# Kernel tuning notes

Measured on AMD Instinct MI355X. Metric: run time of the kernel, lower is better.

Reference implementation:

```python
import jax, jax.numpy as jnp
import numpy as np

N_PARENT = 16384
N_CHILD = 8 * N_PARENT  # nearest upsample, nempty=False: 8 children per parent
C = 128
K = 27  # 3x3x3 octree conv stencil


def setup_inputs() -> dict:
    key = jax.random.key(0)
    k1, k2, k3, k4 = jax.random.split(key, 4)
    x = jax.random.normal(k1, (N_PARENT, C), dtype=jnp.float32)
    # conv weight per stencil offset, fan-in scaled init
    w = jax.random.normal(k2, (K, C, C), dtype=jnp.float32) / np.sqrt(K * C)
    b = jnp.zeros((C,), dtype=jnp.float32)
    # neighbor table at depth+1; -1 marks missing neighbors (zero-padded)
    neigh = jax.random.randint(k3, (N_CHILD, K), -1, N_CHILD, dtype=jnp.int32)
    return {"x": x, "w": w, "b": b, "neigh": neigh}


def reference(x, w, b, neigh):
    # OctreeUpsample(nearest, nempty=False): copy each parent feature to its
    # 8 contiguous children at depth+1.
    xu = jnp.repeat(x, 8, axis=0)  # [N_child, C]
    # OctreeConv: gather 27 neighbors (missing -> 0), then GEMM + bias.
    valid = neigh >= 0  # [N_child, 27]
    g = jnp.where(valid[..., None], xu[jnp.clip(neigh, 0)], 0.0)  # [N_child, 27, C]
    out = jnp.einsum('nkc,kcd->nd', g, w) + b  # [N_child, C]
    return out
```

## Files before the change

kernel.cpp:

```cpp
#include <hip/hip_runtime.h>
#include <hip/hip_bf16.h>

#define N_PARENT 16384
#define N_CHILD (8 * N_PARENT)
#define CC 128
#define KK 27

#define BM 256
#define BN 128
#define BK 32

#define XB_OFF 0
#define XB_ELEMS (N_PARENT * CC)
#define WT_OFF XB_ELEMS
#define WT_ELEMS (KK * CC * CC)
#define ZR_OFF (WT_OFF + WT_ELEMS)
#define ZR_ELEMS 128
#define ZR_ROW 19840

typedef __attribute__((ext_vector_type(8))) __bf16 bf16x8;
typedef __attribute__((ext_vector_type(4))) float f32x4;

__device__ __forceinline__ void gll16(const void* g, void* l) {
  __builtin_amdgcn_global_load_lds(
      (const __attribute__((address_space(1))) unsigned int*)g,
      (__attribute__((address_space(3))) unsigned int*)l,
      16, 0, 0);
}

__global__ void prep_kernel(const float* __restrict__ x,
                            const float* __restrict__ w,
                            __hip_bfloat16* __restrict__ ws) {
  const int stride = gridDim.x * blockDim.x;
  const int tid = blockIdx.x * blockDim.x + threadIdx.x;
  for (int i = tid; i < XB_ELEMS; i += stride)
    ws[XB_OFF + i] = __float2bfloat16(x[i]);
  for (int j = tid; j < WT_ELEMS; j += stride) {
    const int k = j / (CC * CC);
    const int rem = j - k * CC * CC;
    const int d = rem >> 7;
    const int c = rem & 127;
    ws[WT_OFF + j] = __float2bfloat16(w[k * CC * CC + c * CC + d]);
  }
  if (tid < ZR_ELEMS) ws[ZR_OFF + tid] = __float2bfloat16(0.0f);
}

__global__ __launch_bounds__(256, 2) void upconv_kernel(
    const int* __restrict__ neigh,
    const __hip_bfloat16* __restrict__ ws,
    const float* __restrict__ bias,
    float* __restrict__ out) {
  __shared__ __align__(16) __hip_bfloat16 As[2][BM * BK];
  __shared__ __align__(16) __hip_bfloat16 Bs[2][BN * BK];
  __shared__ unsigned short ridx[BM * KK];

  const int tid = threadIdx.x;
  const int wv = tid >> 6;
  const int l = tid & 63;
  const int wr = wv >> 1;
  const int wc = wv & 1;
  const int row0 = blockIdx.x * BM;

  for (int j = tid; j < BM * KK; j += 256) {
    const int nv = neigh[row0 * KK + j];
    ridx[j] = (unsigned short)((nv >= 0) ? (nv >> 3) : ZR_ROW);
  }
  __syncthreads();

  const int lr = l & 15;
  const int coE = (((l >> 4) ^ ((lr >> 1) & 3)) * 8);
  const int lch = ((l & 3) ^ ((l >> 3) & 3)) * 16;

  const char* xbB = (const char*)(ws + XB_OFF);
  const char* wLane =
      (const char*)(ws + WT_OFF) + (wv * 32 + (l >> 2)) * 256 + lch;

  f32x4 acc[8][4] = {};

  const int riB = (wv * 64 + (l >> 2)) * KK;
  int rr[4], nr[4];
#pragma unroll
  for (int i = 0; i < 4; ++i) rr[i] = ((int)ridx[riB + i * 16 * KK]) << 8;

  auto stageA = [&](int buf, int qb, const int* r) {
#pragma unroll
    for (int i = 0; i < 4; ++i)
      gll16(xbB + r[i] + qb + lch, &As[buf][(wv * 64 + i * 16) * BK]);
  };
  auto stageB = [&](int buf, int tqb) {
#pragma unroll
    for (int j = 0; j < 2; ++j)
      gll16(wLane + tqb + j * 4096, &Bs[buf][(wv * 32 + j * 16) * BK]);
  };

  auto compute = [&](int buf) {
    bf16x8 a[8], b[4];
#pragma unroll
    for (int m = 0; m < 8; ++m)
      a[m] = *reinterpret_cast<const bf16x8*>(
          &As[buf][(wr * 128 + m * 16 + lr) * BK + coE]);
#pragma unroll
    for (int n = 0; n < 4; ++n)
      b[n] = *reinterpret_cast<const bf16x8*>(
          &Bs[buf][(wc * 64 + n * 16 + lr) * BK + coE]);
    __builtin_amdgcn_s_setprio(1);
#pragma unroll
    for (int m = 0; m < 8; ++m)
#pragma unroll
      for (int n = 0; n < 4; ++n)
        acc[m][n] = __builtin_amdgcn_mfma_f32_16x16x32_bf16(
            a[m], b[n], acc[m][n], 0, 0, 0);
    __builtin_amdgcn_s_setprio(0);
  };

#define WAITN(n) asm volatile("s_waitcnt vmcnt(" #n ")" ::: "memory")
#define BAR() __builtin_amdgcn_s_barrier()

  stageB(0, 0);
  stageA(0, 0, rr);

  for (int k = 0; k < KK; ++k) {
    const int tb = k * 32768;

    stageB(1, tb + 64);
    stageA(1, 64, rr);
    WAITN(6); BAR();
    compute(0);
    BAR();

    stageB(0, tb + 128);
    stageA(0, 128, rr);
    WAITN(6); BAR();
    compute(1);
    BAR();

    stageB(1, tb + 192);
    stageA(1, 192, rr);
#pragma unroll
    for (int i = 0; i < 4; ++i)
      nr[i] = (k + 1 < KK) ? (((int)ridx[riB + i * 16 * KK + k + 1]) << 8)
                           : rr[i];
    WAITN(6); BAR();
    compute(0);
    BAR();

    if (k + 1 < KK) {
      stageB(0, tb + 32768);
      stageA(0, 0, nr);
      WAITN(6);
    } else {
      WAITN(0);
    }
    BAR();
    compute(1);
    BAR();

#pragma unroll
    for (int i = 0; i < 4; ++i) rr[i] = nr[i];
  }

  float bv[4];
#pragma unroll
  for (int n = 0; n < 4; ++n) bv[n] = bias[wc * 64 + n * 16 + lr];
  const int rbase = row0 + wr * 128 + (l >> 4) * 4;
#pragma unroll
  for (int m = 0; m < 8; ++m)
#pragma unroll
    for (int n = 0; n < 4; ++n)
#pragma unroll
      for (int q = 0; q < 4; ++q)
        out[(size_t)(rbase + m * 16 + q) * CC + wc * 64 + n * 16 + lr] =
            acc[m][n][q] + bv[n];
}

extern "C" void kernel_launch(void* const* d_in, const int* in_sizes, int n_in,
                              void* d_out, int out_size, void* d_ws,
                              size_t ws_size, hipStream_t stream) {
  const float* x = (const float*)d_in[0];
  const float* w = (const float*)d_in[1];
  const float* b = (const float*)d_in[2];
  const int* neigh = (const int*)d_in[3];
  __hip_bfloat16* ws = (__hip_bfloat16*)d_ws;
  float* out = (float*)d_out;

  hipLaunchKernelGGL(prep_kernel, dim3(512), dim3(256), 0, stream, x, w, ws);
  hipLaunchKernelGGL(upconv_kernel, dim3(N_CHILD / BM), dim3(256), 0, stream,
                     neigh, ws, b, out);
}
```

Measured before the change: 129.5 us.

## Precompute per-parent products for all stencil offsets, then gather-sum per child

Computes x_parent·W_k for every parent and all 27 offsets in a dense GEMM (8x fewer rows than children), storing bf16 partial products in workspace. A gather kernel then sums the 27 neighbour partials plus bias per child. This trades most of the MFMA work for a large intermediate write and a random-access gather. It also adds an extra bf16 rounding of partial products, and runs only when the workspace is big enough.

```diff
diff --git a/kernel.cpp b/kernel.cpp
--- a/kernel.cpp
+++ b/kernel.cpp
@@ -17,6 +17,11 @@
 #define ZR_OFF (WT_OFF + WT_ELEMS)
 #define ZR_ELEMS 128
 #define ZR_ROW 19840
+#define PZ_OFF (ZR_OFF + ZR_ELEMS)
+#define PZ_ELEMS (KK * CC)
+#define P_OFF (PZ_OFF + PZ_ELEMS)
+#define P_ELEMS ((size_t)N_PARENT * KK * CC)
+#define NCOL (KK * CC)
 
 typedef __attribute__((ext_vector_type(8))) __bf16 bf16x8;
 typedef __attribute__((ext_vector_type(4))) float f32x4;
@@ -30,7 +35,7 @@
 
 __global__ void prep_kernel(const float* __restrict__ x,
                             const float* __restrict__ w,
-                            __hip_bfloat16* __restrict__ ws) {
+                            __hip_bfloat16* __restrict__ ws, int zero_pz) {
   const int stride = gridDim.x * blockDim.x;
   const int tid = blockIdx.x * blockDim.x + threadIdx.x;
   for (int i = tid; i < XB_ELEMS; i += stride)
@@ -43,6 +48,122 @@
     ws[WT_OFF + j] = __float2bfloat16(w[k * CC * CC + c * CC + d]);
   }
   if (tid < ZR_ELEMS) ws[ZR_OFF + tid] = __float2bfloat16(0.0f);
+  if (zero_pz && tid < PZ_ELEMS) ws[PZ_OFF + tid] = __float2bfloat16(0.0f);
+}
+
+__global__ __launch_bounds__(256, 3) void pgemm_kernel(
+    const __hip_bfloat16* __restrict__ ws, __hip_bfloat16* __restrict__ Pout) {
+  __shared__ __align__(16) __hip_bfloat16 As[2][BM * BK];
+  __shared__ __align__(16) __hip_bfloat16 Bs[2][BN * BK];
+
+  const int tid = threadIdx.x;
+  const int wv = tid >> 6, l = tid & 63;
+  const int wr = wv >> 1, wc = wv & 1;
+  const int bm = blockIdx.x & 63;
+  const int bn = blockIdx.x >> 6;
+  const int row0 = bm * BM;
+
+  const int lr = l & 15;
+  const int coE = ((l >> 4) ^ ((lr >> 1) & 3)) * 8;
+  const int lch = ((l & 3) ^ ((l >> 3) & 3)) * 16;
+
+  const char* aLane = (const char*)(ws + XB_OFF) +
+                      (size_t)(row0 + wv * 64 + (l >> 2)) * 256 + lch;
+  const char* wLane = (const char*)(ws + WT_OFF) + bn * 32768 +
+                      (wv * 32 + (l >> 2)) * 256 + lch;
+
+  f32x4 acc[8][4] = {};
+
+  auto stageAB = [&](int buf, int qb) {
+#pragma unroll
+    for (int i = 0; i < 4; ++i)
+      gll16(aLane + i * 4096 + qb, &As[buf][(wv * 64 + i * 16) * BK]);
+#pragma unroll
+    for (int j = 0; j < 2; ++j)
+      gll16(wLane + j * 4096 + qb, &Bs[buf][(wv * 32 + j * 16) * BK]);
+  };
+  auto compute = [&](int buf) {
+    bf16x8 a[8], b[4];
+#pragma unroll
+    for (int m = 0; m < 8; ++m)
+      a[m] = *reinterpret_cast<const bf16x8*>(
+          &As[buf][(wr * 128 + m * 16 + lr) * BK + coE]);
+#pragma unroll
+    for (int n = 0; n < 4; ++n)
+      b[n] = *reinterpret_cast<const bf16x8*>(
+          &Bs[buf][(wc * 64 + n * 16 + lr) * BK + coE]);
+#pragma unroll
+    for (int m = 0; m < 8; ++m)
+#pragma unroll
+      for (int n = 0; n < 4; ++n)
+        acc[m][n] = __builtin_amdgcn_mfma_f32_16x16x32_bf16(a[m], b[n],
+                                                            acc[m][n], 0, 0, 0);
+  };
+
+#define WAITN(n) asm volatile("s_waitcnt vmcnt(" #n ")" ::: "memory")
+#define BAR() __builtin_amdgcn_s_barrier()
+
+  stageAB(0, 0);
+#pragma unroll
+  for (int q = 0; q < 4; ++q) {
+    if (q + 1 < 4) {
+      stageAB((q + 1) & 1, (q + 1) * 64);
+      WAITN(6);
+    } else {
+      WAITN(0);
+    }
+    BAR();
+    compute(q & 1);
+    BAR();
+  }
+
+  const int prow = row0 + wr * 128 + (l >> 4) * 4;
+  const int pcol = bn * 128 + wc * 64;
+#pragma unroll
+  for (int m = 0; m < 8; ++m)
+#pragma unroll
+    for (int n = 0; n < 4; ++n)
+#pragma unroll
+      for (int q = 0; q < 4; ++q)
+        Pout[(size_t)(prow + m * 16 + q) * NCOL + pcol + n * 16 + lr] =
+            __float2bfloat16(acc[m][n][q]);
+}
+
+__global__ __launch_bounds__(256, 8) void gather_kernel(
+    const int* __restrict__ neigh, const __hip_bfloat16* __restrict__ ws,
+    const float* __restrict__ bias, float* __restrict__ out) {
+  const int tid = threadIdx.x;
+  const int child = blockIdx.x * 16 + (tid >> 4);
+  const int ln = tid & 15;
+  const int d0 = ln * 8;
+
+  const __hip_bfloat16* P = ws + P_OFF;
+  const __hip_bfloat16* PZ = ws + PZ_OFF;
+
+  float a[8];
+  {
+    f32x4 b0 = *reinterpret_cast<const f32x4*>(bias + d0);
+    f32x4 b1 = *reinterpret_cast<const f32x4*>(bias + d0 + 4);
+#pragma unroll
+    for (int j = 0; j < 4; ++j) { a[j] = b0[j]; a[4 + j] = b1[j]; }
+  }
+
+  const int* nrow = neigh + child * KK;
+#pragma unroll 9
+  for (int k = 0; k < KK; ++k) {
+    const int nv = nrow[k];
+    const __hip_bfloat16* src =
+        (nv >= 0) ? (P + (size_t)(nv >> 3) * NCOL + k * 128) : (PZ + k * 128);
+    bf16x8 v = *reinterpret_cast<const bf16x8*>(src + d0);
+#pragma unroll
+    for (int j = 0; j < 8; ++j) a[j] += (float)v[j];
+  }
+
+  float* op = out + (size_t)child * 128 + d0;
+  f32x4 o0 = {a[0], a[1], a[2], a[3]};
+  f32x4 o1 = {a[4], a[5], a[6], a[7]};
+  *reinterpret_cast<f32x4*>(op) = o0;
+  *reinterpret_cast<f32x4*>(op + 4) = o1;
 }
 
 __global__ __launch_bounds__(256, 2) void upconv_kernel(
@@ -92,7 +213,6 @@
     for (int j = 0; j < 2; ++j)
       gll16(wLane + tqb + j * 4096, &Bs[buf][(wv * 32 + j * 16) * BK]);
   };
-
   auto compute = [&](int buf) {
     bf16x8 a[8], b[4];
 #pragma unroll
@@ -108,13 +228,10 @@
     for (int m = 0; m < 8; ++m)
 #pragma unroll
       for (int n = 0; n < 4; ++n)
-        acc[m][n] = __builtin_amdgcn_mfma_f32_16x16x32_bf16(
-            a[m], b[n], acc[m][n], 0, 0, 0);
+        acc[m][n] = __builtin_amdgcn_mfma_f32_16x16x32_bf16(a[m], b[n],
+                                                            acc[m][n], 0, 0, 0);
     __builtin_amdgcn_s_setprio(0);
   };
-
-#define WAITN(n) asm volatile("s_waitcnt vmcnt(" #n ")" ::: "memory")
-#define BAR() __builtin_amdgcn_s_barrier()
 
   stageB(0, 0);
   stageA(0, 0, rr);
@@ -183,7 +300,18 @@
   __hip_bfloat16* ws = (__hip_bfloat16*)d_ws;
   float* out = (float*)d_out;
 
-  hipLaunchKernelGGL(prep_kernel, dim3(512), dim3(256), 0, stream, x, w, ws);
-  hipLaunchKernelGGL(upconv_kernel, dim3(N_CHILD / BM), dim3(256), 0, stream,
-                     neigh, ws, b, out);
-}
+  const size_t need = ((size_t)P_OFF + P_ELEMS) * sizeof(__hip_bfloat16);
+  if (ws_size >= need) {
+    hipLaunchKernelGGL(prep_kernel, dim3(512), dim3(256), 0, stream, x, w, ws,
+                       1);
+    hipLaunchKernelGGL(pgemm_kernel, dim3(64 * KK), dim3(256), 0, stream, ws,
+                       ws + P_OFF);
+    hipLaunchKernelGGL(gather_kernel, dim3(N_CHILD / 16), dim3(256), 0, stream,
+                       neigh, ws, b, out);
+  } else {
+    hipLaunchKernelGGL(prep_kernel, dim3(512), dim3(256), 0, stream, x, w, ws,
+                       0);
+    hipLaunchKernelGGL(upconv_kernel, dim3(N_CHILD / BM), dim3(256), 0, stream,
+                       neigh, ws, b, out);
+  }
+}
```

New measurement: 185.2 us. 43.0% more time.

## Software-pipeline LDS fragment reads with MFMA using double-buffered register fragments

Applied to the files above, without the earlier changes.

Splits the compute step into an LDS fragment read and an MFMA phase, keeping two register fragment buffers. The next tile's fragments are read from shared memory while the current tile's MFMAs run, so LDS latency hides behind matrix math. The loop is rotated to match, with a prologue and an epilogue stage. This raises register pressure (two copies of the A and B fragments) under launch_bounds(256,2), and the buffer-reuse ordering across barriers becomes more delicate.

```diff
diff --git a/kernel.cpp b/kernel.cpp
--- a/kernel.cpp
+++ b/kernel.cpp
@@ -76,6 +76,7 @@
       (const char*)(ws + WT_OFF) + (wv * 32 + (l >> 2)) * 256 + lch;
 
   f32x4 acc[8][4] = {};
+  bf16x8 aR[2][8], bR[2][4];
 
   const int riB = (wv * 64 + (l >> 2)) * KK;
   int rr[4], nr[4];
@@ -93,46 +94,51 @@
       gll16(wLane + tqb + j * 4096, &Bs[buf][(wv * 32 + j * 16) * BK]);
   };
 
-  auto compute = [&](int buf) {
-    bf16x8 a[8], b[4];
+  auto fragRead = [&](int pb, int buf) {
 #pragma unroll
     for (int m = 0; m < 8; ++m)
-      a[m] = *reinterpret_cast<const bf16x8*>(
+      aR[pb][m] = *reinterpret_cast<const bf16x8*>(
           &As[buf][(wr * 128 + m * 16 + lr) * BK + coE]);
 #pragma unroll
     for (int n = 0; n < 4; ++n)
-      b[n] = *reinterpret_cast<const bf16x8*>(
+      bR[pb][n] = *reinterpret_cast<const bf16x8*>(
           &Bs[buf][(wc * 64 + n * 16 + lr) * BK + coE]);
+  };
+
+  auto mfma32 = [&](int pb) {
     __builtin_amdgcn_s_setprio(1);
 #pragma unroll
     for (int m = 0; m < 8; ++m)
 #pragma unroll
       for (int n = 0; n < 4; ++n)
         acc[m][n] = __builtin_amdgcn_mfma_f32_16x16x32_bf16(
-            a[m], b[n], acc[m][n], 0, 0, 0);
+            aR[pb][m], bR[pb][n], acc[m][n], 0, 0, 0);
     __builtin_amdgcn_s_setprio(0);
   };
 
 #define WAITN(n) asm volatile("s_waitcnt vmcnt(" #n ")" ::: "memory")
+#define LGKM0 asm volatile("s_waitcnt lgkmcnt(0)" ::: "memory")
 #define BAR() __builtin_amdgcn_s_barrier()
 
   stageB(0, 0);
   stageA(0, 0, rr);
+  stageB(1, 64);
+  stageA(1, 64, rr);
+  WAITN(6);
+  __syncthreads();
+  fragRead(0, 0);
+  LGKM0;
+  BAR();
 
   for (int k = 0; k < KK; ++k) {
     const int tb = k * 32768;
-
-    stageB(1, tb + 64);
-    stageA(1, 64, rr);
-    WAITN(6); BAR();
-    compute(0);
-    BAR();
 
     stageB(0, tb + 128);
     stageA(0, 128, rr);
     WAITN(6); BAR();
-    compute(1);
-    BAR();
+    fragRead(1, 1);
+    mfma32(0);
+    LGKM0; BAR();
 
     stageB(1, tb + 192);
     stageA(1, 192, rr);
@@ -141,8 +147,9 @@
       nr[i] = (k + 1 < KK) ? (((int)ridx[riB + i * 16 * KK + k + 1]) << 8)
                            : rr[i];
     WAITN(6); BAR();
-    compute(0);
-    BAR();
+    fragRead(0, 0);
+    mfma32(1);
+    LGKM0; BAR();
 
     if (k + 1 < KK) {
       stageB(0, tb + 32768);
@@ -152,8 +159,20 @@
       WAITN(0);
     }
     BAR();
-    compute(1);
-    BAR();
+    fragRead(1, 1);
+    mfma32(0);
+    LGKM0; BAR();
+
+    if (k + 1 < KK) {
+      stageB(1, tb + 32768 + 64);
+      stageA(1, 64, nr);
+      WAITN(6); BAR();
+      fragRead(0, 0);
+      mfma32(1);
+      LGKM0; BAR();
+    } else {
+      mfma32(1);
+    }
 
 #pragma unroll
     for (int i = 0; i < 4; ++i) rr[i] = nr[i];
```

Result: slower. 145.5 us (+12.3%).
